# Performance work log

Measured on AMD Instinct MI355X. Metric: run time of the kernel, lower is better.

## Reference

```python
import jax, jax.numpy as jnp
import numpy as np

NUM_EXPERTS = 8
TOP_K = 2


def setup_inputs() -> dict:
    key = jax.random.key(0)
    k1, k2, k3, k4, k5 = jax.random.split(key, 5)
    B, S, H, I, E = 2, 2048, 1024, 3584, NUM_EXPERTS
    scale_h = 1.0 / np.sqrt(H)
    scale_i = 1.0 / np.sqrt(I)
    return {
        "hidden_states": jax.random.normal(k1, (B, S, H), dtype=jnp.float32),
        "gate_w": jax.random.normal(k2, (H, E), dtype=jnp.float32) * scale_h,
        "w1": jax.random.normal(k3, (E, H, I), dtype=jnp.float32) * scale_h,
        "w3": jax.random.normal(k4, (E, H, I), dtype=jnp.float32) * scale_h,
        "w2": jax.random.normal(k5, (E, I, H), dtype=jnp.float32) * scale_i,
    }


def reference(hidden_states, gate_w, w1, w3, w2):
    # Router: [B,S,H] @ [H,E] -> [B,S,E]
    router_logits = jnp.einsum("bsh,he->bse", hidden_states, gate_w).astype(jnp.float32)
    routing_weights, selected_experts = jax.lax.top_k(router_logits, k=TOP_K)
    routing_weights = jax.nn.softmax(routing_weights, axis=-1)  # [B,S,TOP_K]

    final_hidden_state = jnp.zeros_like(hidden_states)
    # Dense loop over all experts (faithful to the original mask-multiply-accumulate)
    for index in range(NUM_EXPERTS):
        h1 = jax.nn.silu(jnp.einsum("bsh,hi->bsi", hidden_states, w1[index]))
        h3 = jnp.einsum("bsh,hi->bsi", hidden_states, w3[index])
        expert_out = jnp.einsum("bsi,ih->bsh", h1 * h3, w2[index])
        # Per-token routing weight for this expert (0 if not selected)
        weight = jnp.sum(
            jnp.where(selected_experts == index, routing_weights, 0.0), axis=-1
        )[:, :, None]  # [B,S,1]
        final_hidden_state = final_hidden_state + weight * expert_out
    return final_hidden_state, router_logits
```

## Files before the change

### kernel.cpp

```cpp
#include <hip/hip_runtime.h>


typedef __bf16 v8bf __attribute__((ext_vector_type(8)));
typedef float  v4f  __attribute__((ext_vector_type(4)));

constexpr int kT = 4096;
constexpr int kH = 1024;
constexpr int kI = 3584;
constexpr int kE = 8;

constexpr size_t SZ_W    = (size_t)kE * kI * kH * 2;
constexpr size_t OFF_W1T = 0;
constexpr size_t OFF_W3T = OFF_W1T + SZ_W;
constexpr size_t OFF_W2T = OFF_W3T + SZ_W;
constexpr size_t OFF_XG  = OFF_W2T + SZ_W;
constexpr size_t OFF_ACT = OFF_XG  + (size_t)2*kT*kH*2;
constexpr size_t OFF_BUF = OFF_ACT + (size_t)2*kT*kI*2;
constexpr size_t OFF_CNT = OFF_BUF + (size_t)2*kT*kH*4;
constexpr size_t OFF_OFS = OFF_CNT + 128;
constexpr size_t OFF_LST = OFF_OFS + 128;
constexpr size_t OFF_TW  = OFF_LST + (size_t)kE*kT*4;
constexpr size_t OFF_TR  = OFF_TW  + (size_t)kT*2*4;

__device__ __forceinline__ void async16(void* lds, const void* g) {
    __builtin_amdgcn_global_load_lds(
        (const __attribute__((address_space(1))) unsigned int*)g,
        (__attribute__((address_space(3))) unsigned int*)lds,
        16, 0, 0);
}

__global__ void zero_counts_kernel(int* __restrict__ counts) {
    if (threadIdx.x < kE) counts[threadIdx.x] = 0;
}

__global__ void prefix_kernel(const int* __restrict__ counts, int* __restrict__ offsets) {
    if (threadIdx.x == 0) {
        int o = 0;
        for (int e = 0; e < kE; e++) { offsets[e] = o; o += counts[e]; }
    }
}

__global__ void router_kernel(const float* __restrict__ x, const float* __restrict__ gw,
                              float* __restrict__ logits_out, float* __restrict__ tw,
                              int* __restrict__ counts, int* __restrict__ list) {
    const int wave = threadIdx.x >> 6;
    const int lane = threadIdx.x & 63;
    const int t = blockIdx.x * 4 + wave;
    const float* xr = x + (size_t)t * kH;

    double acc[kE];
#pragma unroll
    for (int e = 0; e < kE; e++) acc[e] = 0.0;

    for (int j = 0; j < kH / 64; j++) {
        const int h = j * 64 + lane;
        const float xv = xr[h];
        const float* g = gw + (size_t)h * kE;
#pragma unroll
        for (int e = 0; e < kE; e++) acc[e] += (double)xv * (double)g[e];
    }
#pragma unroll
    for (int e = 0; e < kE; e++) {
#pragma unroll
        for (int o = 32; o > 0; o >>= 1) acc[e] += __shfl_xor(acc[e], o, 64);
    }

    if (lane == 0) {
        float lg[kE];
#pragma unroll
        for (int e = 0; e < kE; e++) lg[e] = (float)acc[e];
#pragma unroll
        for (int e = 0; e < kE; e++) logits_out[(size_t)t * kE + e] = lg[e];

        int e0 = 0; float l0 = lg[0];
        for (int e = 1; e < kE; e++) if (lg[e] > l0) { l0 = lg[e]; e0 = e; }
        int e1 = -1; float l1 = -3.4e38f;
        for (int e = 0; e < kE; e++) if (e != e0 && lg[e] > l1) { l1 = lg[e]; e1 = e; }

        const float ex = __expf(l1 - l0);
        const float w0 = 1.0f / (1.0f + ex);
        const float w1 = ex / (1.0f + ex);

        int s0 = atomicAdd(&counts[e0], 1);
        list[e0 * kT + s0] = t * 2 + 0;
        tw[t * 2 + 0] = w0;
        int s1 = atomicAdd(&counts[e1], 1);
        list[e1 * kT + s1] = t * 2 + 1;
        tw[t * 2 + 1] = w1;
    }
}

__global__ void gather_kernel(const float* __restrict__ x, const int* __restrict__ list,
                              const int* __restrict__ counts, const int* __restrict__ offsets,
                              __bf16* __restrict__ xg, int* __restrict__ trow) {
    const int e = blockIdx.y, s = blockIdx.x;
    if (s >= counts[e]) return;
    const int entry = list[e * kT + s];
    const int t = entry >> 1;
    const int g = offsets[e] + s;
    if (threadIdx.x == 0) trow[entry] = g;
    const int i = threadIdx.x * 4;
    const float4 v = *(const float4*)&x[(size_t)t * kH + i];
    __bf16* d = &xg[(size_t)g * kH + i];
    d[0] = (__bf16)v.x; d[1] = (__bf16)v.y; d[2] = (__bf16)v.z; d[3] = (__bf16)v.w;
}

__global__ void transpose_cvt_kernel(const float* __restrict__ src, __bf16* __restrict__ dst,
                                     int R, int C) {
    __shared__ float tile[32][33];
    const float* s = src + (size_t)blockIdx.z * R * C;
    __bf16* d = dst + (size_t)blockIdx.z * R * C;
    const int c0 = blockIdx.x * 32, r0 = blockIdx.y * 32;
    const int tx = threadIdx.x, ty = threadIdx.y;
#pragma unroll
    for (int i = 0; i < 4; i++)
        tile[ty + i * 8][tx] = s[(size_t)(r0 + ty + i * 8) * C + c0 + tx];
    __syncthreads();
#pragma unroll
    for (int i = 0; i < 4; i++)
        d[(size_t)(c0 + ty + i * 8) * R + r0 + tx] = (__bf16)tile[tx][ty + i * 8];
}

__global__ __launch_bounds__(256, 2) void gemm1_kernel(
    const __bf16* __restrict__ xg, const __bf16* __restrict__ w1t,
    const __bf16* __restrict__ w3t, __bf16* __restrict__ act,
    const int* __restrict__ counts, const int* __restrict__ offsets) {
    const int e = blockIdx.z;
    const int cnt = counts[e];
    const int m0 = blockIdx.y * 128;
    if (m0 >= cnt) return;
    const int n0 = blockIdx.x * 128;
    const int off = offsets[e];

    __shared__ __bf16 As[128 * 32], B1s[128 * 32], B3s[128 * 32];

    const int tid = threadIdx.x;
    const int lane = tid & 63, wave = tid >> 6;
    const int wm = (wave >> 1) * 64, wn = (wave & 1) * 64;
    const int lrow = lane & 15, quad = lane >> 4;

    const int acol = (tid & 3) * 8;
    const __bf16* abase[2];
    const __bf16* b1base[2];
    const __bf16* b3base[2];
    const __bf16* w1b = w1t + (size_t)e * kI * kH + (size_t)n0 * kH;
    const __bf16* w3b = w3t + (size_t)e * kI * kH + (size_t)n0 * kH;
#pragma unroll
    for (int p = 0; p < 2; p++) {
        const int r = p * 64 + (tid >> 2);
        const int gr = min(m0 + r, cnt - 1);
        abase[p]  = xg + (size_t)(off + gr) * kH + acol;
        b1base[p] = w1b + (size_t)r * kH + acol;
        b3base[p] = w3b + (size_t)r * kH + acol;
    }

    v4f acc1[4][4], acc3[4][4];
#pragma unroll
    for (int i = 0; i < 4; i++)
#pragma unroll
        for (int j = 0; j < 4; j++) { acc1[i][j] = (v4f)0.0f; acc3[i][j] = (v4f)0.0f; }

    for (int kt = 0; kt < kH / 32; kt++) {
        const int k0 = kt * 32;
#pragma unroll
        for (int p = 0; p < 2; p++) {
            const int soff = p * 2048 + tid * 8;
            async16(&As[soff],  abase[p]  + k0);
            async16(&B1s[soff], b1base[p] + k0);
            async16(&B3s[soff], b3base[p] + k0);
        }
        __syncthreads();

        v8bf a[4];
#pragma unroll
        for (int fm = 0; fm < 4; fm++)
            a[fm] = *(const v8bf*)&As[(wm + fm * 16 + lrow) * 32 + quad * 8];
#pragma unroll
        for (int fn = 0; fn < 4; fn++) {
            const v8bf b1 = *(const v8bf*)&B1s[(wn + fn * 16 + lrow) * 32 + quad * 8];
            const v8bf b3 = *(const v8bf*)&B3s[(wn + fn * 16 + lrow) * 32 + quad * 8];
#pragma unroll
            for (int fm = 0; fm < 4; fm++) {
                acc1[fm][fn] = __builtin_amdgcn_mfma_f32_16x16x32_bf16(a[fm], b1, acc1[fm][fn], 0, 0, 0);
                acc3[fm][fn] = __builtin_amdgcn_mfma_f32_16x16x32_bf16(a[fm], b3, acc3[fm][fn], 0, 0, 0);
            }
        }
        __syncthreads();
    }

#pragma unroll
    for (int fm = 0; fm < 4; fm++) {
#pragma unroll
        for (int fn = 0; fn < 4; fn++) {
            const v4f c1 = acc1[fm][fn], c3 = acc3[fm][fn];
            const int col = n0 + wn + fn * 16 + lrow;
#pragma unroll
            for (int r = 0; r < 4; r++) {
                const int gm = m0 + wm + fm * 16 + quad * 4 + r;
                if (gm < cnt) {
                    const float h1 = c1[r], h3 = c3[r];
                    const float v = h1 / (1.0f + __expf(-h1)) * h3;
                    act[(size_t)(off + gm) * kI + col] = (__bf16)v;
                }
            }
        }
    }
}

__global__ __launch_bounds__(256, 2) void gemm2_kernel(
    const __bf16* __restrict__ act, const __bf16* __restrict__ w2t,
    float* __restrict__ buf,
    const int* __restrict__ counts, const int* __restrict__ offsets) {
    const int e = blockIdx.z;
    const int cnt = counts[e];
    const int m0 = blockIdx.y * 128;
    if (m0 >= cnt) return;
    const int n0 = blockIdx.x * 128;
    const int off = offsets[e];

    __shared__ __bf16 As[128 * 32], Bs[128 * 32];

    const int tid = threadIdx.x;
    const int lane = tid & 63, wave = tid >> 6;
    const int wm = (wave >> 1) * 64, wn = (wave & 1) * 64;
    const int lrow = lane & 15, quad = lane >> 4;

    const int acol = (tid & 3) * 8;
    const __bf16* abase[2];
    const __bf16* bbase[2];
    const __bf16* w2b = w2t + (size_t)e * kH * kI + (size_t)n0 * kI;
#pragma unroll
    for (int p = 0; p < 2; p++) {
        const int r = p * 64 + (tid >> 2);
        const int gr = min(m0 + r, cnt - 1);
        abase[p] = act + (size_t)(off + gr) * kI + acol;
        bbase[p] = w2b + (size_t)r * kI + acol;
    }

    v4f acc[4][4];
#pragma unroll
    for (int i = 0; i < 4; i++)
#pragma unroll
        for (int j = 0; j < 4; j++) acc[i][j] = (v4f)0.0f;

    for (int kt = 0; kt < kI / 32; kt++) {
        const int k0 = kt * 32;
#pragma unroll
        for (int p = 0; p < 2; p++) {
            const int soff = p * 2048 + tid * 8;
            async16(&As[soff], abase[p] + k0);
            async16(&Bs[soff], bbase[p] + k0);
        }
        __syncthreads();

        v8bf a[4];
#pragma unroll
        for (int fm = 0; fm < 4; fm++)
            a[fm] = *(const v8bf*)&As[(wm + fm * 16 + lrow) * 32 + quad * 8];
#pragma unroll
        for (int fn = 0; fn < 4; fn++) {
            const v8bf b = *(const v8bf*)&Bs[(wn + fn * 16 + lrow) * 32 + quad * 8];
#pragma unroll
            for (int fm = 0; fm < 4; fm++)
                acc[fm][fn] = __builtin_amdgcn_mfma_f32_16x16x32_bf16(a[fm], b, acc[fm][fn], 0, 0, 0);
        }
        __syncthreads();
    }

#pragma unroll
    for (int fm = 0; fm < 4; fm++) {
#pragma unroll
        for (int fn = 0; fn < 4; fn++) {
            const v4f c = acc[fm][fn];
            const int col = n0 + wn + fn * 16 + lrow;
#pragma unroll
            for (int r = 0; r < 4; r++) {
                const int gm = m0 + wm + fm * 16 + quad * 4 + r;
                if (gm < cnt) buf[(size_t)(off + gm) * kH + col] = c[r];
            }
        }
    }
}

__global__ void combine_kernel(const float* __restrict__ buf, const int* __restrict__ trow,
                               const float* __restrict__ tw, float* __restrict__ out) {
    const int t = blockIdx.x;
    const int r0 = trow[2 * t], r1 = trow[2 * t + 1];
    const float w0 = tw[2 * t], w1 = tw[2 * t + 1];
    const int i = threadIdx.x * 4;
    const float4 a = *(const float4*)&buf[(size_t)r0 * kH + i];
    const float4 b = *(const float4*)&buf[(size_t)r1 * kH + i];
    float4 o;
    o.x = w0 * a.x + w1 * b.x;
    o.y = w0 * a.y + w1 * b.y;
    o.z = w0 * a.z + w1 * b.z;
    o.w = w0 * a.w + w1 * b.w;
    *(float4*)&out[(size_t)t * kH + i] = o;
}

extern "C" void kernel_launch(void* const* d_in, const int* in_sizes, int n_in,
                              void* d_out, int out_size, void* d_ws, size_t ws_size,
                              hipStream_t stream) {
    const float* x  = (const float*)d_in[0];
    const float* gw = (const float*)d_in[1];
    const float* w1 = (const float*)d_in[2];
    const float* w3 = (const float*)d_in[3];
    const float* w2 = (const float*)d_in[4];
    float* out = (float*)d_out;
    float* logits_out = out + (size_t)kT * kH;

    char* ws = (char*)d_ws;
    __bf16* w1t   = (__bf16*)(ws + OFF_W1T);
    __bf16* w3t   = (__bf16*)(ws + OFF_W3T);
    __bf16* w2t   = (__bf16*)(ws + OFF_W2T);
    __bf16* xg    = (__bf16*)(ws + OFF_XG);
    __bf16* act   = (__bf16*)(ws + OFF_ACT);
    float*  buf   = (float*) (ws + OFF_BUF);
    int*    cnt   = (int*)   (ws + OFF_CNT);
    int*    ofs   = (int*)   (ws + OFF_OFS);
    int*    list  = (int*)   (ws + OFF_LST);
    float*  tw    = (float*) (ws + OFF_TW);
    int*    trow  = (int*)   (ws + OFF_TR);

    zero_counts_kernel<<<1, 64, 0, stream>>>(cnt);

    transpose_cvt_kernel<<<dim3(kI / 32, kH / 32, kE), dim3(32, 8), 0, stream>>>(w1, w1t, kH, kI);
    transpose_cvt_kernel<<<dim3(kI / 32, kH / 32, kE), dim3(32, 8), 0, stream>>>(w3, w3t, kH, kI);
    transpose_cvt_kernel<<<dim3(kH / 32, kI / 32, kE), dim3(32, 8), 0, stream>>>(w2, w2t, kI, kH);

    router_kernel<<<kT / 4, 256, 0, stream>>>(x, gw, logits_out, tw, cnt, list);
    prefix_kernel<<<1, 1, 0, stream>>>(cnt, ofs);
    gather_kernel<<<dim3(kT, kE), 256, 0, stream>>>(x, list, cnt, ofs, xg, trow);

    gemm1_kernel<<<dim3(kI / 128, kT / 128, kE), 256, 0, stream>>>(xg, w1t, w3t, act, cnt, ofs);
    gemm2_kernel<<<dim3(kH / 128, kT / 128, kE), 256, 0, stream>>>(act, w2t, buf, cnt, ofs);

    combine_kernel<<<kT, 256, 0, stream>>>(buf, trow, tw, out);
}
```

Before: 795.5 us.

## Swizzle GEMM LDS tiles, widen transpose tiles, and compact gather grid

Applies an XOR swizzle to the 16-byte chunk column used for async global-to-LDS loads and MFMA fragment reads in both expert GEMMs, to reduce LDS bank conflicts. The weight transpose-convert kernel moves to 64x64 tiles with float4 loads and packed bf16 stores, and w1/w3 are merged into one launch. The gather kernel now launches exactly 2*kT blocks and finds the expert by scanning offsets, instead of launching kT*kE blocks where most exit early. The swizzle must match between the store and load sides, and the 64x65 float tile raises shared memory per block.

```diff
diff --git a/kernel.cpp b/kernel.cpp
--- a/kernel.cpp
+++ b/kernel.cpp
@@ -93,32 +93,47 @@
 __global__ void gather_kernel(const float* __restrict__ x, const int* __restrict__ list,
                               const int* __restrict__ counts, const int* __restrict__ offsets,
                               __bf16* __restrict__ xg, int* __restrict__ trow) {
-    const int e = blockIdx.y, s = blockIdx.x;
-    if (s >= counts[e]) return;
+    const int g = blockIdx.x;
+    int e = 0;
+    while (e < kE - 1 && g >= offsets[e] + counts[e]) e++;
+    const int s = g - offsets[e];
     const int entry = list[e * kT + s];
     const int t = entry >> 1;
-    const int g = offsets[e] + s;
     if (threadIdx.x == 0) trow[entry] = g;
     const int i = threadIdx.x * 4;
     const float4 v = *(const float4*)&x[(size_t)t * kH + i];
-    __bf16* d = &xg[(size_t)g * kH + i];
-    d[0] = (__bf16)v.x; d[1] = (__bf16)v.y; d[2] = (__bf16)v.z; d[3] = (__bf16)v.w;
-}
-
-__global__ void transpose_cvt_kernel(const float* __restrict__ src, __bf16* __restrict__ dst,
-                                     int R, int C) {
-    __shared__ float tile[32][33];
-    const float* s = src + (size_t)blockIdx.z * R * C;
-    __bf16* d = dst + (size_t)blockIdx.z * R * C;
-    const int c0 = blockIdx.x * 32, r0 = blockIdx.y * 32;
-    const int tx = threadIdx.x, ty = threadIdx.y;
-#pragma unroll
-    for (int i = 0; i < 4; i++)
-        tile[ty + i * 8][tx] = s[(size_t)(r0 + ty + i * 8) * C + c0 + tx];
+    __bf16 pk[4] = {(__bf16)v.x, (__bf16)v.y, (__bf16)v.z, (__bf16)v.w};
+    *(ushort4*)&xg[(size_t)g * kH + i] = *(const ushort4*)pk;
+}
+
+__global__ void transpose_cvt_kernel(const float* __restrict__ srcA, const float* __restrict__ srcB,
+                                     __bf16* __restrict__ dstA, __bf16* __restrict__ dstB,
+                                     int R, int C, int nz) {
+    __shared__ float tile[64][65];
+    const int z = blockIdx.z;
+    const float* s;
+    __bf16* d;
+    if (z < nz) { s = srcA + (size_t)z * R * C;        d = dstA + (size_t)z * R * C; }
+    else        { s = srcB + (size_t)(z - nz) * R * C; d = dstB + (size_t)(z - nz) * R * C; }
+    const int r0 = blockIdx.y * 64, c0 = blockIdx.x * 64;
+    const int tr = threadIdx.x >> 4;
+    const int tc = (threadIdx.x & 15) * 4;
+#pragma unroll
+    for (int i = 0; i < 4; i++) {
+        const float4 v = *(const float4*)&s[(size_t)(r0 + tr + i * 16) * C + (c0 + tc)];
+        tile[tr + i * 16][tc + 0] = v.x;
+        tile[tr + i * 16][tc + 1] = v.y;
+        tile[tr + i * 16][tc + 2] = v.z;
+        tile[tr + i * 16][tc + 3] = v.w;
+    }
     __syncthreads();
 #pragma unroll
-    for (int i = 0; i < 4; i++)
-        d[(size_t)(c0 + ty + i * 8) * R + r0 + tx] = (__bf16)tile[tx][ty + i * 8];
+    for (int i = 0; i < 4; i++) {
+        const int oc = tr + i * 16;
+        __bf16 pk[4] = {(__bf16)tile[tc + 0][oc], (__bf16)tile[tc + 1][oc],
+                        (__bf16)tile[tc + 2][oc], (__bf16)tile[tc + 3][oc]};
+        *(ushort4*)&d[(size_t)(c0 + oc) * R + r0 + tc] = *(const ushort4*)pk;
+    }
 }
 
 __global__ __launch_bounds__(256, 2) void gemm1_kernel(
@@ -139,7 +154,7 @@
     const int wm = (wave >> 1) * 64, wn = (wave & 1) * 64;
     const int lrow = lane & 15, quad = lane >> 4;
 
-    const int acol = (tid & 3) * 8;
+    const int scol = (((tid & 3) ^ ((tid >> 2) & 3) ^ ((tid >> 4) & 3))) * 8;
     const __bf16* abase[2];
     const __bf16* b1base[2];
     const __bf16* b3base[2];
@@ -149,10 +164,13 @@
     for (int p = 0; p < 2; p++) {
         const int r = p * 64 + (tid >> 2);
         const int gr = min(m0 + r, cnt - 1);
-        abase[p]  = xg + (size_t)(off + gr) * kH + acol;
-        b1base[p] = w1b + (size_t)r * kH + acol;
-        b3base[p] = w3b + (size_t)r * kH + acol;
-    }
+        abase[p]  = xg + (size_t)(off + gr) * kH + scol;
+        b1base[p] = w1b + (size_t)r * kH + scol;
+        b3base[p] = w3b + (size_t)r * kH + scol;
+    }
+
+    const int sw = (lane & 3) ^ ((lane >> 2) & 3);
+    const int fragoff = lrow * 32 + ((quad ^ sw) * 8);
 
     v4f acc1[4][4], acc3[4][4];
 #pragma unroll
@@ -174,11 +192,11 @@
         v8bf a[4];
 #pragma unroll
         for (int fm = 0; fm < 4; fm++)
-            a[fm] = *(const v8bf*)&As[(wm + fm * 16 + lrow) * 32 + quad * 8];
+            a[fm] = *(const v8bf*)&As[(wm + fm * 16) * 32 + fragoff];
 #pragma unroll
         for (int fn = 0; fn < 4; fn++) {
-            const v8bf b1 = *(const v8bf*)&B1s[(wn + fn * 16 + lrow) * 32 + quad * 8];
-            const v8bf b3 = *(const v8bf*)&B3s[(wn + fn * 16 + lrow) * 32 + quad * 8];
+            const v8bf b1 = *(const v8bf*)&B1s[(wn + fn * 16) * 32 + fragoff];
+            const v8bf b3 = *(const v8bf*)&B3s[(wn + fn * 16) * 32 + fragoff];
 #pragma unroll
             for (int fm = 0; fm < 4; fm++) {
                 acc1[fm][fn] = __builtin_amdgcn_mfma_f32_16x16x32_bf16(a[fm], b1, acc1[fm][fn], 0, 0, 0);
@@ -225,7 +243,7 @@
     const int wm = (wave >> 1) * 64, wn = (wave & 1) * 64;
     const int lrow = lane & 15, quad = lane >> 4;
 
-    const int acol = (tid & 3) * 8;
+    const int scol = (((tid & 3) ^ ((tid >> 2) & 3) ^ ((tid >> 4) & 3))) * 8;
     const __bf16* abase[2];
     const __bf16* bbase[2];
     const __bf16* w2b = w2t + (size_t)e * kH * kI + (size_t)n0 * kI;
@@ -233,9 +251,12 @@
     for (int p = 0; p < 2; p++) {
         const int r = p * 64 + (tid >> 2);
         const int gr = min(m0 + r, cnt - 1);
-        abase[p] = act + (size_t)(off + gr) * kI + acol;
-        bbase[p] = w2b + (size_t)r * kI + acol;
-    }
+        abase[p] = act + (size_t)(off + gr) * kI + scol;
+        bbase[p] = w2b + (size_t)r * kI + scol;
+    }
+
+    const int sw = (lane & 3) ^ ((lane >> 2) & 3);
+    const int fragoff = lrow * 32 + ((quad ^ sw) * 8);
 
     v4f acc[4][4];
 #pragma unroll
@@ -256,10 +277,10 @@
         v8bf a[4];
 #pragma unroll
         for (int fm = 0; fm < 4; fm++)
-            a[fm] = *(const v8bf*)&As[(wm + fm * 16 + lrow) * 32 + quad * 8];
+            a[fm] = *(const v8bf*)&As[(wm + fm * 16) * 32 + fragoff];
 #pragma unroll
         for (int fn = 0; fn < 4; fn++) {
-            const v8bf b = *(const v8bf*)&Bs[(wn + fn * 16 + lrow) * 32 + quad * 8];
+            const v8bf b = *(const v8bf*)&Bs[(wn + fn * 16) * 32 + fragoff];
 #pragma unroll
             for (int fm = 0; fm < 4; fm++)
                 acc[fm][fn] = __builtin_amdgcn_mfma_f32_16x16x32_bf16(a[fm], b, acc[fm][fn], 0, 0, 0);
@@ -324,13 +345,14 @@
 
     zero_counts_kernel<<<1, 64, 0, stream>>>(cnt);
 
-    transpose_cvt_kernel<<<dim3(kI / 32, kH / 32, kE), dim3(32, 8), 0, stream>>>(w1, w1t, kH, kI);
-    transpose_cvt_kernel<<<dim3(kI / 32, kH / 32, kE), dim3(32, 8), 0, stream>>>(w3, w3t, kH, kI);
-    transpose_cvt_kernel<<<dim3(kH / 32, kI / 32, kE), dim3(32, 8), 0, stream>>>(w2, w2t, kI, kH);
+    transpose_cvt_kernel<<<dim3(kI / 64, kH / 64, 2 * kE), 256, 0, stream>>>(
+        w1, w3, w1t, w3t, kH, kI, kE);
+    transpose_cvt_kernel<<<dim3(kH / 64, kI / 64, kE), 256, 0, stream>>>(
+        w2, w2, w2t, w2t, kI, kH, kE);
 
     router_kernel<<<kT / 4, 256, 0, stream>>>(x, gw, logits_out, tw, cnt, list);
     prefix_kernel<<<1, 1, 0, stream>>>(cnt, ofs);
-    gather_kernel<<<dim3(kT, kE), 256, 0, stream>>>(x, list, cnt, ofs, xg, trow);
+    gather_kernel<<<2 * kT, 256, 0, stream>>>(x, list, cnt, ofs, xg, trow);
 
     gemm1_kernel<<<dim3(kI / 128, kT / 128, kE), 256, 0, stream>>>(xg, w1t, w3t, act, cnt, ofs);
     gemm2_kernel<<<dim3(kH / 128, kT / 128, kE), 256, 0, stream>>>(act, w2t, buf, cnt, ofs);
```

Result: no change. 788.0 us (-0.9%).
